# Kernel optimization log

Hardware: AMD Instinct MI355X
Metric: run time of the kernel (lower is better)

## Reference

```python
import jax, jax.numpy as jnp
import numpy as np

NODES_PER_GRAPH = 1430  # hard-coded stride in the original forward
GENE0 = 1421            # first gene node index per graph
N_HEADS = 9


def gcn_conv(x, W, b, src, dst, n):
    """PyG-style GCNConv: D^-1/2 (A+I) D^-1/2 X W + b (self-loops added)."""
    h = x @ W  # [N, out]
    ones = jnp.ones(src.shape, jnp.float32)
    deg = jax.ops.segment_sum(ones, dst, num_segments=n) + 1.0  # +1 self-loop
    dinv = jax.lax.rsqrt(deg)
    norm = dinv[src] * dinv[dst]  # [E]
    agg = jax.ops.segment_sum(norm[:, None] * h[src], dst, num_segments=n)
    agg = agg + (dinv * dinv)[:, None] * h  # self-loop contribution
    return agg + b


def setup_inputs() -> dict:
    key = jax.random.key(0)
    ks = jax.random.split(key, 8)
    n_graphs = 512
    n = NODES_PER_GRAPH * n_graphs  # 732160 nodes
    e = n * 8                        # avg degree 8
    x = jax.random.normal(ks[0], (n, 1), jnp.float32)
    edge_index = jax.random.randint(ks[1], (2, e), 0, n, jnp.int32)
    y = jnp.zeros((n_graphs * N_HEADS,), jnp.int32)  # only y.size(0) is used
    W1 = jax.random.normal(ks[2], (1, 16), jnp.float32) * 0.5
    b1 = jnp.zeros((16,), jnp.float32)
    W2 = jax.random.normal(ks[3], (16, 16), jnp.float32) * 0.25
    b2 = jnp.zeros((16,), jnp.float32)
    fw1 = jax.random.normal(ks[4], (N_HEADS, 16, 8), jnp.float32) * 0.25
    fb1 = jnp.zeros((N_HEADS, 8), jnp.float32)
    fw2 = jax.random.normal(ks[5], (N_HEADS, 8, 1), jnp.float32) * 0.35
    fb2 = jnp.zeros((N_HEADS, 1), jnp.float32)
    return {"x": x, "edge_index": edge_index, "y": y, "W1": W1, "b1": b1,
            "W2": W2, "b2": b2, "fw1": fw1, "fb1": fb1, "fw2": fw2, "fb2": fb2}


def reference(x, edge_index, y, W1, b1, W2, b2, fw1, fb1, fw2, fb2):
    n = x.shape[0]
    src, dst = edge_index[0], edge_index[1]
    h = jax.nn.relu(gcn_conv(x, W1, b1, src, dst, n))
    # F.dropout(p=0.4) treated as identity (deterministic eval reference)
    h = jax.nn.relu(gcn_conv(h, W2, b2, src, dst, n))
    n_graphs = y.shape[0] // N_HEADS
    # fused version of the per-gene gather loop: idx[g, k] = 1421+g + k*1430
    idx = (GENE0 + jnp.arange(N_HEADS)[:, None]
           + jnp.arange(n_graphs)[None, :] * NODES_PER_GRAPH)  # [9, G]
    g = h[idx]  # [9, G, 16]
    z = jax.nn.relu(jnp.einsum('gnf,gfh->gnh', g, fw1) + fb1[:, None, :])
    pred = jnp.einsum('gnh,gho->gno', z, fw2) + fb2[:, None, :]  # [9, G, 1]
    return tuple(pred[i] for i in range(N_HEADS))
```

## Files before the change

kernel.cpp:

```cpp
#include <hip/hip_runtime.h>

#define NODES 1430
#define GENE0 1421
#define NHEADS 9
#define BHIST 1024
#define GMAX 64
#define QCAP 1024
#define L1B 1024
#define L1QCAP 3072

__device__ __forceinline__ float frelu(float v) { return v > 0.f ? v : 0.f; }

__global__ __launch_bounds__(BHIST, 4)
void k_hist(const int* __restrict__ esrc, const int* __restrict__ edst,
            unsigned int* __restrict__ copies,
            int* __restrict__ gene_cnt, int* __restrict__ gene_src,
            unsigned int* __restrict__ flagw,
            int e, int K, int R, int n, int hbins, int hwords) {
    extern __shared__ unsigned int lds[];
    int id = blockIdx.x;
    int k, r;
    if ((K & 7) == 0) {
        int xcd = id & 7;
        int slot = id >> 3;
        int cin = slot / R;
        k = xcd * (K >> 3) + cin;
        r = slot - cin * R;
    } else {
        k = id / R;
        r = id - k * R;
    }
    const int tid = threadIdx.x;
    {
        uint4* l4 = (uint4*)lds;
        const int hw4 = hwords >> 2;
        for (int w = tid; w < hw4; w += BHIST) l4[w] = make_uint4(0, 0, 0, 0);
    }
    __syncthreads();

    const unsigned int lo = (unsigned int)r * (unsigned int)hbins;
    const unsigned int hb = (unsigned int)hbins;
    const int e4 = e >> 2;
    const int Q = (e4 + K - 1) / K;
    const int beg = k * Q;
    const int end = min(beg + Q, e4);
    const int4* ed4 = (const int4*)edst;
    const int len = (end > beg) ? (end - beg) : 0;
    const int eighth = len >> 3;

    auto proc = [&](int4 d4, int j4) {
#pragma unroll
        for (int c = 0; c < 4; c++) {
            unsigned int d = (unsigned int)((&d4.x)[c]);
            unsigned int rel = d - lo;
            if (rel < hb) {
                atomicAdd(&lds[rel >> 3], 1u << ((rel & 7u) * 4u));
                unsigned int graph = d / NODES;
                unsigned int pos = d - graph * NODES;
                if (pos >= GENE0) {
                    int s = esrc[4 * j4 + c];
                    atomicOr(&flagw[(unsigned)s >> 5], 1u << (s & 31));
                    int g = (int)(graph * NHEADS + (pos - GENE0));
                    int p = atomicAdd(gene_cnt + g, 1);
                    if (p < GMAX) gene_src[(g << 6) + p] = s;
                }
            }
        }
    };

    for (int i = tid; i < eighth; i += BHIST) {
        int j0 = beg + i;
        int4 v0 = ed4[j0];
        int4 v1 = ed4[j0 + eighth];
        int4 v2 = ed4[j0 + 2 * eighth];
        int4 v3 = ed4[j0 + 3 * eighth];
        int4 v4 = ed4[j0 + 4 * eighth];
        int4 v5 = ed4[j0 + 5 * eighth];
        int4 v6 = ed4[j0 + 6 * eighth];
        int4 v7 = ed4[j0 + 7 * eighth];
        proc(v0, j0);
        proc(v1, j0 + eighth);
        proc(v2, j0 + 2 * eighth);
        proc(v3, j0 + 3 * eighth);
        proc(v4, j0 + 4 * eighth);
        proc(v5, j0 + 5 * eighth);
        proc(v6, j0 + 6 * eighth);
        proc(v7, j0 + 7 * eighth);
    }
    for (int i = (eighth << 3) + tid; i < len; i += BHIST) {
        proc(ed4[beg + i], beg + i);
    }

    if (k == 0) {
        for (int j = (e4 << 2) + tid; j < e; j += BHIST) {
            unsigned int d = (unsigned int)edst[j];
            unsigned int rel = d - lo;
            if (rel < hb) {
                atomicAdd(&lds[rel >> 3], 1u << ((rel & 7u) * 4u));
                unsigned int graph = d / NODES;
                unsigned int pos = d - graph * NODES;
                if (pos >= GENE0) {
                    int s = esrc[j];
                    atomicOr(&flagw[(unsigned)s >> 5], 1u << (s & 31));
                    int g = (int)(graph * NHEADS + (pos - GENE0));
                    int p = atomicAdd(gene_cnt + g, 1);
                    if (p < GMAX) gene_src[(g << 6) + p] = s;
                }
            }
        }
    }
    __syncthreads();
    int wlimit = (n > (int)lo) ? ((n - (int)lo + 7) >> 3) : 0;
    if (wlimit > hwords) wlimit = hwords;
    int w4 = (wlimit + 3) >> 2;
    uint4* dst4 = (uint4*)(copies + ((size_t)k * R + r) * hwords);
    const uint4* l4 = (const uint4*)lds;
    for (int w = tid; w < w4; w += BHIST) dst4[w] = l4[w];
}

__global__ void k_reduce(const unsigned int* __restrict__ copies,
                         const float* __restrict__ x,
                         float2* __restrict__ dx, float* __restrict__ t,
                         unsigned int* __restrict__ flagw,
                         int n, int K, int Wtot) {
    int w = blockIdx.x * blockDim.x + threadIdx.x;
    if (w >= Wtot) return;
    int i0 = w << 3;
    if (i0 >= n) return;
    const unsigned int M = 0x0F0F0F0Fu;
    unsigned int ev[8] = {0, 0, 0, 0, 0, 0, 0, 0};
    unsigned int od[8] = {0, 0, 0, 0, 0, 0, 0, 0};
    int k = 0;
    for (; k + 8 <= K; k += 8) {
#pragma unroll
        for (int s = 0; s < 8; s++) {
            unsigned int u = copies[(size_t)(k + s) * Wtot + w];
            ev[s] += u & M; od[s] += (u >> 4) & M;
        }
    }
    for (; k < K; k++) {
        unsigned int u = copies[(size_t)k * Wtot + w];
        ev[0] += u & M; od[0] += (u >> 4) & M;
    }
    unsigned int evn = ((ev[0] + ev[1]) + (ev[2] + ev[3])) + ((ev[4] + ev[5]) + (ev[6] + ev[7]));
    unsigned int odd = ((od[0] + od[1]) + (od[2] + od[3])) + ((od[4] + od[5]) + (od[6] + od[7]));
    float v[8];
#pragma unroll
    for (int b = 0; b < 4; b++) {
        v[2 * b]     = (float)((evn >> (8 * b)) & 0xFFu);
        v[2 * b + 1] = (float)((odd >> (8 * b)) & 0xFFu);
    }
#pragma unroll
    for (int b = 0; b < 8; b++) v[b] = rsqrtf(v[b] + 1.f);
    float4 z4 = {0.f, 0.f, 0.f, 0.f};
    if (i0 + 7 < n) {
        float4 xa = *(const float4*)(x + i0);
        float4 xb = *(const float4*)(x + i0 + 4);
        float4 p0 = {v[0], v[0] * xa.x, v[1], v[1] * xa.y};
        float4 p1 = {v[2], v[2] * xa.z, v[3], v[3] * xa.w};
        float4 p2 = {v[4], v[4] * xb.x, v[5], v[5] * xb.y};
        float4 p3 = {v[6], v[6] * xb.z, v[7], v[7] * xb.w};
        float4* dst = (float4*)(dx + i0);
        dst[0] = p0; dst[1] = p1; dst[2] = p2; dst[3] = p3;
        *(float4*)(t + i0) = z4;
        *(float4*)(t + i0 + 4) = z4;
    } else {
        for (int b = 0; b < 8; b++)
            if (i0 + b < n) {
                float xv = x[i0 + b];
                dx[i0 + b] = make_float2(v[b], v[b] * xv);
                t[i0 + b] = 0.f;
            }
    }
#pragma unroll
    for (int b = 0; b < 8; b++) {
        int i = i0 + b;
        if (i < n) {
            unsigned int graph = (unsigned int)i / NODES;
            unsigned int pos = (unsigned int)i - graph * NODES;
            if (pos >= GENE0) atomicOr(&flagw[(unsigned)i >> 5], 1u << (i & 31));
        }
    }
}

__global__ __launch_bounds__(L1B, 4)
void k_l1_scatter_lds(const int* __restrict__ esrc, const int* __restrict__ edst,
                      const float2* __restrict__ dx,
                      const unsigned int* __restrict__ flagw,
                      float* __restrict__ t, int e, int nw) {
    extern __shared__ unsigned int sh[];
    unsigned int* fl = sh;
    int2* q = (int2*)(sh + ((nw + 3) & ~3));
    __shared__ int qn;
    const int tid = threadIdx.x;
    if (tid == 0) qn = 0;
    {
        const uint4* g4 = (const uint4*)flagw;
        uint4* l4 = (uint4*)fl;
        int nw4 = nw >> 2;
        for (int w = tid; w < nw4; w += L1B) l4[w] = g4[w];
        for (int w = (nw4 << 2) + tid; w < nw; w += L1B) fl[w] = flagw[w];
    }
    __syncthreads();

    const int e4 = e >> 2;
    const int nb = gridDim.x;
    const int Q = (e4 + nb - 1) / nb;
    const int beg = blockIdx.x * Q;
    const int end = min(beg + Q, e4);
    const int len = (end > beg) ? (end - beg) : 0;
    const int4* ed4 = (const int4*)edst;

    auto test = [&](int4 dd, int j4) {
#pragma unroll
        for (int c = 0; c < 4; c++) {
            int d = (&dd.x)[c];
            if ((fl[(unsigned)d >> 5] >> (d & 31)) & 1u) {
                int p = atomicAdd(&qn, 1);
                if (p < L1QCAP) q[p] = make_int2(4 * j4 + c, d);
                else atomicAdd(t + d, dx[esrc[4 * j4 + c]].y);
            }
        }
    };

    const int quarter = len >> 2;
    for (int i = tid; i < quarter; i += L1B) {
        int j0 = beg + i;
        int4 d0 = ed4[j0];
        int4 d1 = ed4[j0 + quarter];
        int4 d2 = ed4[j0 + 2 * quarter];
        int4 d3 = ed4[j0 + 3 * quarter];
        test(d0, j0);
        test(d1, j0 + quarter);
        test(d2, j0 + 2 * quarter);
        test(d3, j0 + 3 * quarter);
    }
    for (int i = (quarter << 2) + tid; i < len; i += L1B) {
        test(ed4[beg + i], beg + i);
    }
    if (blockIdx.x == 0) {
        for (int j = (e4 << 2) + tid; j < e; j += L1B) {
            int d = edst[j];
            if ((fl[(unsigned)d >> 5] >> (d & 31)) & 1u)
                atomicAdd(t + d, dx[esrc[j]].y);
        }
    }
    __syncthreads();
    int m = min(qn, L1QCAP);
    for (int i = tid; i < m; i += L1B) {
        int2 jd = q[i];
        q[i].x = esrc[jd.x];
    }
    __syncthreads();
    for (int i = tid; i < m; i += L1B) {
        int2 sd = q[i];
        atomicAdd(t + sd.y, dx[sd.x].y);
    }
}

__global__ __launch_bounds__(256, 8)
void k_l1_scatter_g(const int* __restrict__ esrc, const int* __restrict__ edst,
                    const float2* __restrict__ dx,
                    const unsigned int* __restrict__ flagw,
                    float* __restrict__ t, int e) {
    __shared__ int2 q[QCAP];
    __shared__ int qn;
    const int tid = threadIdx.x;
    if (tid == 0) qn = 0;
    __syncthreads();

    const int4* ed4 = (const int4*)edst;
    const int4* es4 = (const int4*)esrc;
    const int e4 = e >> 2;
    const int g0 = blockIdx.x * 512;
#pragma unroll
    for (int u = 0; u < 2; u++) {
        int gi = g0 + u * 256 + tid;
        if (gi < e4) {
            int4 dd = ed4[gi];
            int4 ss = es4[gi];
#pragma unroll
            for (int c = 0; c < 4; c++) {
                int d = (&dd.x)[c];
                if ((flagw[(unsigned)d >> 5] >> (d & 31)) & 1u) {
                    int p = atomicAdd(&qn, 1);
                    if (p < QCAP) q[p] = make_int2((&ss.x)[c], d);
                    else atomicAdd(t + d, dx[(&ss.x)[c]].y);
                }
            }
        }
    }
    if (blockIdx.x == 0) {
        for (int j = (e4 << 2) + tid; j < e; j += 256) {
            int d = edst[j];
            if ((flagw[(unsigned)d >> 5] >> (d & 31)) & 1u) {
                int s = esrc[j];
                atomicAdd(t + d, dx[s].y);
            }
        }
    }
    __syncthreads();
    int m = min(qn, QCAP);
    for (int i = tid; i < m; i += 256) {
        int2 sd = q[i];
        atomicAdd(t + sd.y, dx[sd.x].y);
    }
}

__global__ void k_gene_final(const int* __restrict__ gene_cnt, const int* __restrict__ gene_src,
                             const float* __restrict__ t, const float2* __restrict__ dx,
                             const float* __restrict__ W1, const float* __restrict__ b1,
                             const float* __restrict__ W2, const float* __restrict__ b2,
                             const float* __restrict__ fw1, const float* __restrict__ fb1,
                             const float* __restrict__ fw2, const float* __restrict__ fb2,
                             float* __restrict__ out, int NG, int G) {
    int wid = (blockIdx.x * blockDim.x + threadIdx.x) >> 6;
    int lane = threadIdx.x & 63;
    if (wid >= NG) return;
    int g = wid;
    int graph = g / NHEADS;
    int head = g - graph * NHEADS;
    int node = graph * NODES + GENE0 + head;
    const int c = lane & 15;
    const int slot = lane >> 4;

    int cnt = min(gene_cnt[g], GMAX);

    float w1r[16], b1r[16], w2c[16];
#pragma unroll
    for (int kk = 0; kk < 16; kk++) {
        w1r[kk] = W1[kk];
        b1r[kk] = b1[kk];
        w2c[kk] = W2[kk * 16 + c];
    }
    float2 dn2 = dx[node];
    float tn = t[node];

    float acc = 0.f;
    const int base = g << 6;
    for (int i = slot; i < cnt; i += 8) {
        int s0 = gene_src[base + i];
        int i1 = i + 4;
        int s1 = (i1 < cnt) ? gene_src[base + i1] : -1;
        float2 a2 = dx[s0];
        float ta = t[s0];
        float2 b2v = (s1 >= 0) ? dx[s1] : make_float2(0.f, 0.f);
        float tb = (s1 >= 0) ? t[s1] : 0.f;
        {
            float us = a2.x * ta + a2.x * a2.y;
            float m = 0.f;
#pragma unroll
            for (int kk = 0; kk < 16; kk++)
                m += frelu(us * w1r[kk] + b1r[kk]) * w2c[kk];
            acc += a2.x * m;
        }
        if (s1 >= 0) {
            float us = b2v.x * tb + b2v.x * b2v.y;
            float m = 0.f;
#pragma unroll
            for (int kk = 0; kk < 16; kk++)
                m += frelu(us * w1r[kk] + b1r[kk]) * w2c[kk];
            acc += b2v.x * m;
        }
    }
    acc += __shfl_xor(acc, 16, 64);
    acc += __shfl_xor(acc, 32, 64);

    float dn = dn2.x;
    float un = dn * tn + dn * dn2.y;
    float h2 = 0.f;
#pragma unroll
    for (int kk = 0; kk < 16; kk++)
        h2 += frelu(un * w1r[kk] + b1r[kk]) * w2c[kk];
    float h = frelu(dn * acc + dn * dn * h2 + b2[c]);

    float hv[16];
#pragma unroll
    for (int c2 = 0; c2 < 16; c2++) hv[c2] = __shfl(h, c2, 64);

    int kk = lane & 7;
    float z = fb1[head * 8 + kk];
#pragma unroll
    for (int c2 = 0; c2 < 16; c2++) z += hv[c2] * fw1[head * 128 + c2 * 8 + kk];
    float term = frelu(z) * fw2[head * 8 + kk];
    term += __shfl_xor(term, 1, 64);
    term += __shfl_xor(term, 2, 64);
    term += __shfl_xor(term, 4, 64);
    if (lane == 0) out[head * G + graph] = fb2[head] + term;
}

extern "C" void kernel_launch(void* const* d_in, const int* in_sizes, int n_in,
                              void* d_out, int out_size, void* d_ws, size_t ws_size,
                              hipStream_t stream) {
    const float* x   = (const float*)d_in[0];
    const int*   ei  = (const int*)d_in[1];
    const float* W1  = (const float*)d_in[3];
    const float* b1  = (const float*)d_in[4];
    const float* W2  = (const float*)d_in[5];
    const float* b2  = (const float*)d_in[6];
    const float* fw1 = (const float*)d_in[7];
    const float* fb1 = (const float*)d_in[8];
    const float* fw2 = (const float*)d_in[9];
    const float* fb2 = (const float*)d_in[10];

    int n = in_sizes[0];
    int e = in_sizes[1] / 2;
    int G = in_sizes[2] / NHEADS;
    int NG = G * NHEADS;
    const int* esrc = ei;
    const int* edst = ei + e;

    int nw = (n + 31) / 32;
    size_t l1_shmem = (size_t)((nw + 3) & ~3) * 4 + (size_t)L1QCAP * 8;

    static int HB_RT = 0;
    static int L1_LDS_OK = 0;
    if (HB_RT == 0) {
        hipError_t st = hipFuncSetAttribute(
            reinterpret_cast<const void*>(k_hist),
            hipFuncAttributeMaxDynamicSharedMemorySize, 131072);
        HB_RT = (st == hipSuccess) ? 262144 : 131072;
        hipError_t st2 = hipFuncSetAttribute(
            reinterpret_cast<const void*>(k_l1_scatter_lds),
            hipFuncAttributeMaxDynamicSharedMemorySize, (int)l1_shmem);
        L1_LDS_OK = (st2 == hipSuccess && l1_shmem <= 160 * 1024) ? 1 : -1;
    }
    const int HB = HB_RT;
    const int HW = HB >> 3;

    char* ws = (char*)d_ws;
    size_t off = 0;
    auto alloc = [&](size_t bytes) {
        char* p = ws + off;
        off += (bytes + 255) & ~(size_t)255;
        return p;
    };
    int*   gene_cnt      = (int*)alloc((size_t)NG * 4);
    unsigned int* flagw  = (unsigned int*)alloc((size_t)nw * 4);
    size_t zero_bytes    = off;
    int*    gene_src     = (int*)alloc((size_t)NG * GMAX * 4);
    float*  t            = (float*)alloc((size_t)n * 4);
    float2* dx           = (float2*)alloc((size_t)n * 8);
    size_t fixed         = off;

    int R = (n + HB - 1) / HB;
    size_t per_copy = (size_t)R * HW * 4;
    int K = 80;
    if (fixed + (size_t)K * per_copy > ws_size) {
        size_t avail = (ws_size > fixed) ? (ws_size - fixed) : 0;
        int kfit = (int)(avail / per_copy);
        if (kfit >= 8) kfit &= ~7;
        K = kfit < 1 ? 1 : (kfit < K ? kfit : K);
    }
    unsigned int* copies = (unsigned int*)alloc((size_t)K * per_copy);
    (void)n_in; (void)out_size;

    hipMemsetAsync(d_ws, 0, zero_bytes, stream);

    const int B = 256;
    size_t shmem = (size_t)HW * 4;
    k_hist<<<K * R, BHIST, shmem, stream>>>(esrc, edst, copies, gene_cnt, gene_src,
                                            flagw, e, K, R, n, HB, HW);
    int Wtot = R * HW;
    k_reduce<<<(Wtot + B - 1) / B, B, 0, stream>>>(copies, x, dx, t, flagw, n, K, Wtot);
    if (L1_LDS_OK == 1) {
        k_l1_scatter_lds<<<256, L1B, l1_shmem, stream>>>(esrc, edst, dx, flagw, t, e, nw);
    } else {
        int nblk = ((e >> 2) + 511) / 512;
        k_l1_scatter_g<<<nblk, 256, 0, stream>>>(esrc, edst, dx, flagw, t, e);
    }
    int waves_blocks = (NG * 64 + B - 1) / B;
    k_gene_final<<<waves_blocks, B, 0, stream>>>(gene_cnt, gene_src, t, dx,
                                                 W1, b1, W2, b2,
                                                 fw1, fb1, fw2, fb2,
                                                 (float*)d_out, NG, G);
}
```

Before: 171.3 us.

## Replace LDS-partitioned degree histogram with direct global atomic degree counts

Drops the multi-copy LDS histogram with 4-bit packed counters and the reduction kernel that summed those copies. Node in-degrees are now counted with a global atomicAdd per edge into a zeroed int array, and a simple kernel turns them into rsqrt normalisers. This removes the repeated edge-stream passes across row ranges and the large copies buffer, but adds about 5.8M scattered global atomics on random addresses plus a memset of the degree array.

```diff
diff --git a/kernel.cpp b/kernel.cpp
--- a/kernel.cpp
+++ b/kernel.cpp
@@ -3,72 +3,47 @@
 #define NODES 1430
 #define GENE0 1421
 #define NHEADS 9
-#define BHIST 1024
 #define GMAX 64
 #define QCAP 1024
 #define L1B 1024
 #define L1QCAP 3072
+#define DEGB 1024
 
 __device__ __forceinline__ float frelu(float v) { return v > 0.f ? v : 0.f; }
 
-__global__ __launch_bounds__(BHIST, 4)
-void k_hist(const int* __restrict__ esrc, const int* __restrict__ edst,
-            unsigned int* __restrict__ copies,
-            int* __restrict__ gene_cnt, int* __restrict__ gene_src,
-            unsigned int* __restrict__ flagw,
-            int e, int K, int R, int n, int hbins, int hwords) {
-    extern __shared__ unsigned int lds[];
-    int id = blockIdx.x;
-    int k, r;
-    if ((K & 7) == 0) {
-        int xcd = id & 7;
-        int slot = id >> 3;
-        int cin = slot / R;
-        k = xcd * (K >> 3) + cin;
-        r = slot - cin * R;
-    } else {
-        k = id / R;
-        r = id - k * R;
-    }
+__global__ __launch_bounds__(DEGB, 2)
+void k_deg(const int* __restrict__ esrc, const int* __restrict__ edst,
+           int* __restrict__ deg,
+           int* __restrict__ gene_cnt, int* __restrict__ gene_src,
+           unsigned int* __restrict__ flagw, int e) {
     const int tid = threadIdx.x;
-    {
-        uint4* l4 = (uint4*)lds;
-        const int hw4 = hwords >> 2;
-        for (int w = tid; w < hw4; w += BHIST) l4[w] = make_uint4(0, 0, 0, 0);
-    }
-    __syncthreads();
-
-    const unsigned int lo = (unsigned int)r * (unsigned int)hbins;
-    const unsigned int hb = (unsigned int)hbins;
     const int e4 = e >> 2;
-    const int Q = (e4 + K - 1) / K;
-    const int beg = k * Q;
+    const int nb = gridDim.x;
+    const int Q = (e4 + nb - 1) / nb;
+    const int beg = blockIdx.x * Q;
     const int end = min(beg + Q, e4);
+    const int len = (end > beg) ? (end - beg) : 0;
     const int4* ed4 = (const int4*)edst;
-    const int len = (end > beg) ? (end - beg) : 0;
     const int eighth = len >> 3;
 
     auto proc = [&](int4 d4, int j4) {
 #pragma unroll
         for (int c = 0; c < 4; c++) {
             unsigned int d = (unsigned int)((&d4.x)[c]);
-            unsigned int rel = d - lo;
-            if (rel < hb) {
-                atomicAdd(&lds[rel >> 3], 1u << ((rel & 7u) * 4u));
-                unsigned int graph = d / NODES;
-                unsigned int pos = d - graph * NODES;
-                if (pos >= GENE0) {
-                    int s = esrc[4 * j4 + c];
-                    atomicOr(&flagw[(unsigned)s >> 5], 1u << (s & 31));
-                    int g = (int)(graph * NHEADS + (pos - GENE0));
-                    int p = atomicAdd(gene_cnt + g, 1);
-                    if (p < GMAX) gene_src[(g << 6) + p] = s;
-                }
+            atomicAdd(&deg[d], 1);
+            unsigned int graph = d / NODES;
+            unsigned int pos = d - graph * NODES;
+            if (pos >= GENE0) {
+                int s = esrc[4 * j4 + c];
+                atomicOr(&flagw[(unsigned)s >> 5], 1u << (s & 31));
+                int g = (int)(graph * NHEADS + (pos - GENE0));
+                int p = atomicAdd(gene_cnt + g, 1);
+                if (p < GMAX) gene_src[(g << 6) + p] = s;
             }
         }
     };
 
-    for (int i = tid; i < eighth; i += BHIST) {
+    for (int i = tid; i < eighth; i += DEGB) {
         int j0 = beg + i;
         int4 v0 = ed4[j0];
         int4 v1 = ed4[j0 + eighth];
@@ -87,75 +62,46 @@
         proc(v6, j0 + 6 * eighth);
         proc(v7, j0 + 7 * eighth);
     }
-    for (int i = (eighth << 3) + tid; i < len; i += BHIST) {
+    for (int i = (eighth << 3) + tid; i < len; i += DEGB) {
         proc(ed4[beg + i], beg + i);
     }
-
-    if (k == 0) {
-        for (int j = (e4 << 2) + tid; j < e; j += BHIST) {
+    if (blockIdx.x == 0) {
+        for (int j = (e4 << 2) + tid; j < e; j += DEGB) {
             unsigned int d = (unsigned int)edst[j];
-            unsigned int rel = d - lo;
-            if (rel < hb) {
-                atomicAdd(&lds[rel >> 3], 1u << ((rel & 7u) * 4u));
-                unsigned int graph = d / NODES;
-                unsigned int pos = d - graph * NODES;
-                if (pos >= GENE0) {
-                    int s = esrc[j];
-                    atomicOr(&flagw[(unsigned)s >> 5], 1u << (s & 31));
-                    int g = (int)(graph * NHEADS + (pos - GENE0));
-                    int p = atomicAdd(gene_cnt + g, 1);
-                    if (p < GMAX) gene_src[(g << 6) + p] = s;
-                }
-            }
-        }
-    }
-    __syncthreads();
-    int wlimit = (n > (int)lo) ? ((n - (int)lo + 7) >> 3) : 0;
-    if (wlimit > hwords) wlimit = hwords;
-    int w4 = (wlimit + 3) >> 2;
-    uint4* dst4 = (uint4*)(copies + ((size_t)k * R + r) * hwords);
-    const uint4* l4 = (const uint4*)lds;
-    for (int w = tid; w < w4; w += BHIST) dst4[w] = l4[w];
-}
-
-__global__ void k_reduce(const unsigned int* __restrict__ copies,
-                         const float* __restrict__ x,
-                         float2* __restrict__ dx, float* __restrict__ t,
-                         unsigned int* __restrict__ flagw,
-                         int n, int K, int Wtot) {
-    int w = blockIdx.x * blockDim.x + threadIdx.x;
-    if (w >= Wtot) return;
-    int i0 = w << 3;
+            atomicAdd(&deg[d], 1);
+            unsigned int graph = d / NODES;
+            unsigned int pos = d - graph * NODES;
+            if (pos >= GENE0) {
+                int s = esrc[j];
+                atomicOr(&flagw[(unsigned)s >> 5], 1u << (s & 31));
+                int g = (int)(graph * NHEADS + (pos - GENE0));
+                int p = atomicAdd(gene_cnt + g, 1);
+                if (p < GMAX) gene_src[(g << 6) + p] = s;
+            }
+        }
+    }
+}
+
+__global__ void k_dx(const int* __restrict__ deg, const float* __restrict__ x,
+                     float2* __restrict__ dx, float* __restrict__ t,
+                     unsigned int* __restrict__ flagw, int n) {
+    int i0 = (blockIdx.x * blockDim.x + threadIdx.x) << 3;
     if (i0 >= n) return;
-    const unsigned int M = 0x0F0F0F0Fu;
-    unsigned int ev[8] = {0, 0, 0, 0, 0, 0, 0, 0};
-    unsigned int od[8] = {0, 0, 0, 0, 0, 0, 0, 0};
-    int k = 0;
-    for (; k + 8 <= K; k += 8) {
-#pragma unroll
-        for (int s = 0; s < 8; s++) {
-            unsigned int u = copies[(size_t)(k + s) * Wtot + w];
-            ev[s] += u & M; od[s] += (u >> 4) & M;
-        }
-    }
-    for (; k < K; k++) {
-        unsigned int u = copies[(size_t)k * Wtot + w];
-        ev[0] += u & M; od[0] += (u >> 4) & M;
-    }
-    unsigned int evn = ((ev[0] + ev[1]) + (ev[2] + ev[3])) + ((ev[4] + ev[5]) + (ev[6] + ev[7]));
-    unsigned int odd = ((od[0] + od[1]) + (od[2] + od[3])) + ((od[4] + od[5]) + (od[6] + od[7]));
-    float v[8];
-#pragma unroll
-    for (int b = 0; b < 4; b++) {
-        v[2 * b]     = (float)((evn >> (8 * b)) & 0xFFu);
-        v[2 * b + 1] = (float)((odd >> (8 * b)) & 0xFFu);
-    }
-#pragma unroll
-    for (int b = 0; b < 8; b++) v[b] = rsqrtf(v[b] + 1.f);
     float4 z4 = {0.f, 0.f, 0.f, 0.f};
     if (i0 + 7 < n) {
+        int4 d0 = *(const int4*)(deg + i0);
+        int4 d1 = *(const int4*)(deg + i0 + 4);
         float4 xa = *(const float4*)(x + i0);
         float4 xb = *(const float4*)(x + i0 + 4);
+        float v[8];
+        v[0] = rsqrtf((float)d0.x + 1.f);
+        v[1] = rsqrtf((float)d0.y + 1.f);
+        v[2] = rsqrtf((float)d0.z + 1.f);
+        v[3] = rsqrtf((float)d0.w + 1.f);
+        v[4] = rsqrtf((float)d1.x + 1.f);
+        v[5] = rsqrtf((float)d1.y + 1.f);
+        v[6] = rsqrtf((float)d1.z + 1.f);
+        v[7] = rsqrtf((float)d1.w + 1.f);
         float4 p0 = {v[0], v[0] * xa.x, v[1], v[1] * xa.y};
         float4 p1 = {v[2], v[2] * xa.z, v[3], v[3] * xa.w};
         float4 p2 = {v[4], v[4] * xb.x, v[5], v[5] * xb.y};
@@ -167,8 +113,8 @@
     } else {
         for (int b = 0; b < 8; b++)
             if (i0 + b < n) {
-                float xv = x[i0 + b];
-                dx[i0 + b] = make_float2(v[b], v[b] * xv);
+                float dv = rsqrtf((float)deg[i0 + b] + 1.f);
+                dx[i0 + b] = make_float2(dv, dv * x[i0 + b]);
                 t[i0 + b] = 0.f;
             }
     }
@@ -413,20 +359,13 @@
     int nw = (n + 31) / 32;
     size_t l1_shmem = (size_t)((nw + 3) & ~3) * 4 + (size_t)L1QCAP * 8;
 
-    static int HB_RT = 0;
     static int L1_LDS_OK = 0;
-    if (HB_RT == 0) {
-        hipError_t st = hipFuncSetAttribute(
-            reinterpret_cast<const void*>(k_hist),
-            hipFuncAttributeMaxDynamicSharedMemorySize, 131072);
-        HB_RT = (st == hipSuccess) ? 262144 : 131072;
+    if (L1_LDS_OK == 0) {
         hipError_t st2 = hipFuncSetAttribute(
             reinterpret_cast<const void*>(k_l1_scatter_lds),
             hipFuncAttributeMaxDynamicSharedMemorySize, (int)l1_shmem);
         L1_LDS_OK = (st2 == hipSuccess && l1_shmem <= 160 * 1024) ? 1 : -1;
     }
-    const int HB = HB_RT;
-    const int HW = HB >> 3;
 
     char* ws = (char*)d_ws;
     size_t off = 0;
@@ -437,32 +376,19 @@
     };
     int*   gene_cnt      = (int*)alloc((size_t)NG * 4);
     unsigned int* flagw  = (unsigned int*)alloc((size_t)nw * 4);
+    int*   deg           = (int*)alloc((size_t)n * 4);
     size_t zero_bytes    = off;
     int*    gene_src     = (int*)alloc((size_t)NG * GMAX * 4);
     float*  t            = (float*)alloc((size_t)n * 4);
     float2* dx           = (float2*)alloc((size_t)n * 8);
-    size_t fixed         = off;
-
-    int R = (n + HB - 1) / HB;
-    size_t per_copy = (size_t)R * HW * 4;
-    int K = 80;
-    if (fixed + (size_t)K * per_copy > ws_size) {
-        size_t avail = (ws_size > fixed) ? (ws_size - fixed) : 0;
-        int kfit = (int)(avail / per_copy);
-        if (kfit >= 8) kfit &= ~7;
-        K = kfit < 1 ? 1 : (kfit < K ? kfit : K);
-    }
-    unsigned int* copies = (unsigned int*)alloc((size_t)K * per_copy);
-    (void)n_in; (void)out_size;
+    (void)n_in; (void)out_size; (void)ws_size;
 
     hipMemsetAsync(d_ws, 0, zero_bytes, stream);
 
     const int B = 256;
-    size_t shmem = (size_t)HW * 4;
-    k_hist<<<K * R, BHIST, shmem, stream>>>(esrc, edst, copies, gene_cnt, gene_src,
-                                            flagw, e, K, R, n, HB, HW);
-    int Wtot = R * HW;
-    k_reduce<<<(Wtot + B - 1) / B, B, 0, stream>>>(copies, x, dx, t, flagw, n, K, Wtot);
+    k_deg<<<512, DEGB, 0, stream>>>(esrc, edst, deg, gene_cnt, gene_src, flagw, e);
+    int nthr = (n + 7) >> 3;
+    k_dx<<<(nthr + B - 1) / B, B, 0, stream>>>(deg, x, dx, t, flagw, n);
     if (L1_LDS_OK == 1) {
         k_l1_scatter_lds<<<256, L1B, l1_shmem, stream>>>(esrc, edst, dx, flagw, t, e, nw);
     } else {
```

New measurement: 367.8 us. 2.15x slower.
